# Kernel tuning notes

Hardware: AMD Instinct MI355X
Metric: run time of the kernel (lower is better)

Reference implementation:

```python
import jax, jax.numpy as jnp
import numpy as np

N_NODES = 50000
N_EDGES = 800000
IN_F, H_F, OUT_F = 512, 128, 64


def _graph_conv(x, W, b, src, dst, norm_src, norm_dst):
    # DGL GraphConv, norm='both': out = D_dst^-1/2 * A * (D_src^-1/2 * x) @ W + b
    # weight applied before aggregation (in_feats >= out_feats path) — math identical.
    h = (x * norm_src[:, None]) @ W                      # [N, out_f]
    agg = jax.ops.segment_sum(h[src], dst, num_segments=N_NODES)  # SpMM gather/scatter
    return agg * norm_dst[:, None] + b


def setup_inputs() -> dict:
    key = jax.random.key(0)
    ks = jax.random.split(key, 12)
    x = jax.random.normal(ks[0], (N_NODES, IN_F), dtype=jnp.float32)
    src = jax.random.randint(ks[1], (N_EDGES,), 0, N_NODES, dtype=jnp.int64)
    dst = jax.random.randint(ks[2], (N_EDGES,), 0, N_NODES, dtype=jnp.int64)

    def glorot(k, fan_in, fan_out):
        s = jnp.sqrt(6.0 / (fan_in + fan_out)).astype(jnp.float32)
        return jax.random.uniform(k, (fan_in, fan_out), jnp.float32, -s, s)

    return {
        'x': x, 'src': src, 'dst': dst,
        'W1': glorot(ks[3], IN_F, H_F), 'b1': jnp.zeros((H_F,), jnp.float32),
        'W2': glorot(ks[4], H_F, H_F), 'b2': jnp.zeros((H_F,), jnp.float32),
        'W3': glorot(ks[5], H_F, H_F), 'b3': jnp.zeros((H_F,), jnp.float32),
        'W4': glorot(ks[6], H_F, OUT_F), 'b4': jnp.zeros((OUT_F,), jnp.float32),
        'embedding_layer': 3,
    }


def reference(x, src, dst, W1, b1, W2, b2, W3, b3, W4, b4, embedding_layer):
    ones = jnp.ones((N_EDGES,), jnp.float32)
    out_deg = jnp.maximum(jax.ops.segment_sum(ones, src, num_segments=N_NODES), 1.0)
    in_deg = jnp.maximum(jax.ops.segment_sum(ones, dst, num_segments=N_NODES), 1.0)
    norm_src = jax.lax.rsqrt(out_deg)
    norm_dst = jax.lax.rsqrt(in_deg)

    h1 = jax.nn.relu(_graph_conv(x, W1, b1, src, dst, norm_src, norm_dst))
    h2 = jax.nn.relu(_graph_conv(h1, W2, b2, src, dst, norm_src, norm_dst))
    h3 = jax.nn.relu(_graph_conv(h2, W3, b3, src, dst, norm_src, norm_dst))
    h4 = _graph_conv(h3, W4, b4, src, dst, norm_src, norm_dst)

    hidden = [h1, h2, h3, h4][embedding_layer - 1]  # embedding_layer is a static int
    return (h4, hidden, x)
```

## Files before the change

kernel.cpp:

```cpp
#include <hip/hip_runtime.h>

#define N_NODES 50000
#define N_EDGES 800000
#define IN_F 512
#define H_F 128
#define OUT_F 64


__global__ void detect_kernel(const void* __restrict__ edges, int* __restrict__ flag) {
    if (threadIdx.x == 0 && blockIdx.x == 0) {
        const long long* p = (const long long*)edges;
        int is64 = 1;
        for (int k = 0; k < 256; k++) {
            long long v = p[k];
            if (v < 0 || v >= N_NODES) { is64 = 0; break; }
        }
        flag[0] = is64;
    }
}

__device__ __forceinline__ int edge_at(const void* __restrict__ p, int e, int is64) {
    return is64 ? (int)((const long long*)p)[e] : ((const int*)p)[e];
}

__global__ void count_kernel(const void* __restrict__ src, const void* __restrict__ dst,
                             int* __restrict__ cs, int* __restrict__ cd,
                             const int* __restrict__ flag) {
    int is64 = flag[0];
    int e = blockIdx.x * 256 + threadIdx.x;
    if (e < N_EDGES) {
        atomicAdd(&cs[edge_at(src, e, is64)], 1);
        atomicAdd(&cd[edge_at(dst, e, is64)], 1);
    }
}

__global__ void scan_kernel(const int* __restrict__ in, int* __restrict__ exc,
                            int* __restrict__ bsums, int n) {
    __shared__ int tmp[1024];
    int tid = threadIdx.x;
    int gid = blockIdx.x * 1024 + tid;
    int v = (gid < n) ? in[gid] : 0;
    tmp[tid] = v;
    __syncthreads();
    for (int off = 1; off < 1024; off <<= 1) {
        int t = (tid >= off) ? tmp[tid - off] : 0;
        __syncthreads();
        tmp[tid] += t;
        __syncthreads();
    }
    if (gid < n) exc[gid] = tmp[tid] - v;
    if (tid == 1023) bsums[blockIdx.x] = tmp[1023];
}

__global__ void finalize_kernel(const int* __restrict__ exc, const int* __restrict__ bexc,
                                int* __restrict__ rp, int* __restrict__ cur,
                                const int* __restrict__ cs, const int* __restrict__ cd,
                                float* __restrict__ ns, float* __restrict__ nd) {
    int i = blockIdx.x * 256 + threadIdx.x;
    if (i < N_NODES) {
        int v = exc[i] + bexc[i >> 10];
        rp[i] = v;
        cur[i] = v;
        if (i == 0) rp[N_NODES] = N_EDGES;
        ns[i] = 1.0f / sqrtf(fmaxf((float)cs[i], 1.0f));
        nd[i] = 1.0f / sqrtf(fmaxf((float)cd[i], 1.0f));
    }
}

__global__ void fill_kernel(const void* __restrict__ src, const void* __restrict__ dst,
                            int* __restrict__ cur, int* __restrict__ col,
                            const int* __restrict__ flag) {
    int is64 = flag[0];
    int e = blockIdx.x * 256 + threadIdx.x;
    if (e < N_EDGES) {
        int d = edge_at(dst, e, is64);
        int pos = atomicAdd(&cur[d], 1);
        col[pos] = edge_at(src, e, is64);
    }
}


__device__ __forceinline__ constexpr int swz(int f) { return f + (f >> 3); }

template <int N, int BM, bool COPY>
__global__ __launch_bounds__(256) void gemm_norm(const float* __restrict__ A, const float* __restrict__ W,
                                                 const float* __restrict__ norm, float* __restrict__ C,
                                                 int K, float* __restrict__ xc) {
    constexpr int TX = N / 8;
    constexpr int TY = 256 / TX;
    constexpr int RT = BM / TY;
    constexpr int NF4 = N / 4;
    constexpr int SA = BM + 4;
    constexpr int SW = (swz(NF4 - 1) + 1) * 4;
    constexpr int APT = BM * 32 / 4 / 256;
    constexpr int WPT = 32 * NF4 / 256;

    __shared__ float Ast[32 * SA];
    __shared__ float Ws[32 * SW];

    const int t = threadIdx.x;
    const int tx = t % TX, ty = t / TX;
    const int m0 = blockIdx.x * BM;
    const int KT = K / 32;

    float4 abuf[APT], wbuf[WPT];

    auto load_tile = [&](int k0) {
        #pragma unroll
        for (int p = 0; p < APT; p++) {
            int idx = t + p * 256;
            int r = idx >> 3;
            int c = (idx & 7) << 2;
            int row = m0 + r;
            abuf[p] = make_float4(0.f, 0.f, 0.f, 0.f);
            if (row < N_NODES) abuf[p] = *(const float4*)&A[(size_t)row * K + k0 + c];
        }
        #pragma unroll
        for (int p = 0; p < WPT; p++) {
            int idx = t + p * 256;
            int r = idx / NF4;
            int f = idx % NF4;
            wbuf[p] = *(const float4*)&W[(size_t)(k0 + r) * N + f * 4];
        }
    };
    auto store_tile = [&](int k0) {
        #pragma unroll
        for (int p = 0; p < APT; p++) {
            int idx = t + p * 256;
            int r = idx >> 3;
            int c = (idx & 7) << 2;
            Ast[(c + 0) * SA + r] = abuf[p].x;
            Ast[(c + 1) * SA + r] = abuf[p].y;
            Ast[(c + 2) * SA + r] = abuf[p].z;
            Ast[(c + 3) * SA + r] = abuf[p].w;
            if (COPY) {
                int row = m0 + r;
                if (row < N_NODES) *(float4*)&xc[(size_t)row * K + k0 + c] = abuf[p];
            }
        }
        #pragma unroll
        for (int p = 0; p < WPT; p++) {
            int idx = t + p * 256;
            int r = idx / NF4;
            int f = idx % NF4;
            *(float4*)&Ws[r * SW + swz(f) * 4] = wbuf[p];
        }
    };

    float acc[RT][8];
    #pragma unroll
    for (int i = 0; i < RT; i++)
        #pragma unroll
        for (int j = 0; j < 8; j++) acc[i][j] = 0.f;

    load_tile(0);
    store_tile(0);
    __syncthreads();

    for (int kt = 0; kt < KT; kt++) {
        if (kt + 1 < KT) load_tile((kt + 1) * 32);
        #pragma unroll 8
        for (int kk = 0; kk < 32; kk++) {
            float a[RT], w[8];
            #pragma unroll
            for (int r4 = 0; r4 < RT / 4; r4++)
                *(float4*)&a[r4 * 4] = *(const float4*)&Ast[kk * SA + ty * RT + r4 * 4];
            int f0 = tx * 2;
            *(float4*)&w[0] = *(const float4*)&Ws[kk * SW + (f0 + (f0 >> 3)) * 4];
            *(float4*)&w[4] = *(const float4*)&Ws[kk * SW + (f0 + 1 + ((f0 + 1) >> 3)) * 4];
            #pragma unroll
            for (int i = 0; i < RT; i++)
                #pragma unroll
                for (int j = 0; j < 8; j++) acc[i][j] = fmaf(a[i], w[j], acc[i][j]);
        }
        __syncthreads();
        if (kt + 1 < KT) {
            store_tile((kt + 1) * 32);
            __syncthreads();
        }
    }

    #pragma unroll
    for (int i = 0; i < RT; i++) {
        int row = m0 + ty * RT + i;
        if (row < N_NODES) {
            float s = norm[row];
            float4 o0 = make_float4(acc[i][0] * s, acc[i][1] * s, acc[i][2] * s, acc[i][3] * s);
            float4 o1 = make_float4(acc[i][4] * s, acc[i][5] * s, acc[i][6] * s, acc[i][7] * s);
            *(float4*)&C[(size_t)row * N + tx * 8] = o0;
            *(float4*)&C[(size_t)row * N + tx * 8 + 4] = o1;
        }
    }
}


template <int FEAT, bool RELU, bool HID>
__global__ __launch_bounds__(256) void spmm_kernel(
        const float* __restrict__ h, const int* __restrict__ rp,
        const int* __restrict__ col, const float* __restrict__ nd,
        const float* __restrict__ bias, float* __restrict__ out,
        float* __restrict__ hid, const int* __restrict__ emb, int layer) {
    int i = blockIdx.x * 4 + (threadIdx.x >> 6);
    i = __builtin_amdgcn_readfirstlane(i);
    if (i >= N_NODES) return;
    int lane = threadIdx.x & 63;
    int beg = rp[i], end = rp[i + 1];

    if constexpr (FEAT == 128) {
        float ax = 0.f, ay = 0.f;
        int e = beg;
        for (; e + 8 <= end; e += 8) {
            int c0 = col[e], c1 = col[e+1], c2 = col[e+2], c3 = col[e+3];
            int c4 = col[e+4], c5 = col[e+5], c6 = col[e+6], c7 = col[e+7];
            float2 v0 = *(const float2*)&h[(size_t)c0 * FEAT + lane * 2];
            float2 v1 = *(const float2*)&h[(size_t)c1 * FEAT + lane * 2];
            float2 v2 = *(const float2*)&h[(size_t)c2 * FEAT + lane * 2];
            float2 v3 = *(const float2*)&h[(size_t)c3 * FEAT + lane * 2];
            float2 v4 = *(const float2*)&h[(size_t)c4 * FEAT + lane * 2];
            float2 v5 = *(const float2*)&h[(size_t)c5 * FEAT + lane * 2];
            float2 v6 = *(const float2*)&h[(size_t)c6 * FEAT + lane * 2];
            float2 v7 = *(const float2*)&h[(size_t)c7 * FEAT + lane * 2];
            ax += (v0.x + v1.x) + (v2.x + v3.x) + ((v4.x + v5.x) + (v6.x + v7.x));
            ay += (v0.y + v1.y) + (v2.y + v3.y) + ((v4.y + v5.y) + (v6.y + v7.y));
        }
        for (; e < end; e++) {
            float2 v = *(const float2*)&h[(size_t)col[e] * FEAT + lane * 2];
            ax += v.x; ay += v.y;
        }
        float s = nd[i];
        float2 b = *(const float2*)&bias[lane * 2];
        float vx = fmaf(ax, s, b.x), vy = fmaf(ay, s, b.y);
        if (RELU) { vx = fmaxf(vx, 0.f); vy = fmaxf(vy, 0.f); }
        float2 o = make_float2(vx, vy);
        *(float2*)&out[(size_t)i * FEAT + lane * 2] = o;
        if (HID) {
            if (emb[0] == layer) *(float2*)&hid[(size_t)i * FEAT + lane * 2] = o;
        }
    } else {
        float acc = 0.f;
        int e = beg;
        for (; e + 8 <= end; e += 8) {
            int c0 = col[e], c1 = col[e+1], c2 = col[e+2], c3 = col[e+3];
            int c4 = col[e+4], c5 = col[e+5], c6 = col[e+6], c7 = col[e+7];
            float v0 = h[(size_t)c0 * FEAT + lane];
            float v1 = h[(size_t)c1 * FEAT + lane];
            float v2 = h[(size_t)c2 * FEAT + lane];
            float v3 = h[(size_t)c3 * FEAT + lane];
            float v4 = h[(size_t)c4 * FEAT + lane];
            float v5 = h[(size_t)c5 * FEAT + lane];
            float v6 = h[(size_t)c6 * FEAT + lane];
            float v7 = h[(size_t)c7 * FEAT + lane];
            acc += (v0 + v1) + (v2 + v3) + ((v4 + v5) + (v6 + v7));
        }
        for (; e < end; e++) acc += h[(size_t)col[e] * FEAT + lane];
        float v = fmaf(acc, nd[i], bias[lane]);
        if (RELU) v = fmaxf(v, 0.f);
        out[(size_t)i * FEAT + lane] = v;
        if (HID) {
            if (emb[0] == layer) hid[(size_t)i * FEAT + lane] = v;
        }
    }
}


extern "C" void kernel_launch(void* const* d_in, const int* in_sizes, int n_in,
                              void* d_out, int out_size, void* d_ws, size_t ws_size,
                              hipStream_t stream) {
    const float* x = (const float*)d_in[0];
    const void* src = d_in[1];
    const void* dst = d_in[2];
    const float* W1 = (const float*)d_in[3];  const float* b1 = (const float*)d_in[4];
    const float* W2 = (const float*)d_in[5];  const float* b2 = (const float*)d_in[6];
    const float* W3 = (const float*)d_in[7];  const float* b3 = (const float*)d_in[8];
    const float* W4 = (const float*)d_in[9];  const float* b4 = (const float*)d_in[10];
    const int* emb = (const int*)d_in[11];
    float* out = (float*)d_out;

    char* w = (char*)d_ws;
    int* cnt_src = (int*)w;  w += 51200 * 4;
    int* cnt_dst = (int*)w;  w += 51200 * 4;
    float* norm_src = (float*)w; w += 51200 * 4;
    float* norm_dst = (float*)w; w += 51200 * 4;
    int* exc = (int*)w;      w += 51200 * 4;
    int* bsums = (int*)w;    w += 1024 * 4;
    int* bexc = (int*)w;     w += 1024 * 4;
    int* bdummy = (int*)w;   w += 1024 * 4;
    int* dflag = (int*)w;    w += 1024 * 4;
    int* rp = (int*)w;       w += 51200 * 4;
    int* cur = (int*)w;      w += 51200 * 4;
    int* col = (int*)w;      w += 800768 * 4;
    float* gbuf = (float*)w; w += (size_t)6400000 * 4;
    float* hbuf = (float*)w; w += (size_t)6400000 * 4;

    hipMemsetAsync(cnt_src, 0, 2 * 51200 * 4, stream);
    detect_kernel<<<1, 64, 0, stream>>>(dst, dflag);
    count_kernel<<<3125, 256, 0, stream>>>(src, dst, cnt_src, cnt_dst, dflag);
    scan_kernel<<<49, 1024, 0, stream>>>(cnt_dst, exc, bsums, N_NODES);
    scan_kernel<<<1, 1024, 0, stream>>>(bsums, bexc, bdummy, 49);
    finalize_kernel<<<196, 256, 0, stream>>>(exc, bexc, rp, cur,
                                             cnt_src, cnt_dst, norm_src, norm_dst);
    fill_kernel<<<3125, 256, 0, stream>>>(src, dst, cur, col, dflag);

    const int GB64 = (N_NODES + 63) / 64;
    const int GB128 = (N_NODES + 127) / 128;
    const int SB = (N_NODES + 3) / 4;
    float* hid = out + (size_t)N_NODES * OUT_F;
    float* xcopy = hid + (size_t)N_NODES * H_F;

    gemm_norm<128, 64, true><<<GB64, 256, 0, stream>>>(x, W1, norm_src, gbuf, IN_F, xcopy);
    spmm_kernel<128, true, true><<<SB, 256, 0, stream>>>(gbuf, rp, col, norm_dst, b1, hbuf, hid, emb, 1);

    gemm_norm<128, 64, false><<<GB64, 256, 0, stream>>>(hbuf, W2, norm_src, gbuf, H_F, nullptr);
    spmm_kernel<128, true, true><<<SB, 256, 0, stream>>>(gbuf, rp, col, norm_dst, b2, hbuf, hid, emb, 2);

    gemm_norm<128, 64, false><<<GB64, 256, 0, stream>>>(hbuf, W3, norm_src, gbuf, H_F, nullptr);
    spmm_kernel<128, true, true><<<SB, 256, 0, stream>>>(gbuf, rp, col, norm_dst, b3, hbuf, hid, emb, 3);

    gemm_norm<64, 128, false><<<GB128, 256, 0, stream>>>(hbuf, W4, norm_src, gbuf, H_F, nullptr);
    spmm_kernel<64, false, false><<<SB, 256, 0, stream>>>(gbuf, rp, col, norm_dst, b4, out, nullptr, nullptr, 0);
}
```

Measured before the change: 754.3 us.

## Replace FP32 SIMT GEMM with split-bf16 MFMA GEMM and pre-swizzled weights

Replaces the scalar FP32 tiled GEMM with an MFMA-based kernel that represents each FP32 value as a bf16 hi/lo pair and uses three bf16 MFMAs per tile to approximate FP32 precision. Weights are converted once per call into hi/lo bf16 arrays laid out in the MFMA operand fragment order. Activations are split on the fly and staged through a small shared-memory tile. This trades FP32 FMA throughput for matrix-core throughput, at the cost of reduced precision and a smaller 32-row tile that does less data reuse and syncs twice per K step.

Result: faster. 648.6 us (-14.0%).

```diff
diff --git a/kernel.cpp b/kernel.cpp
--- a/kernel.cpp
+++ b/kernel.cpp
@@ -80,115 +80,113 @@
 }
 
 
-__device__ __forceinline__ constexpr int swz(int f) { return f + (f >> 3); }
-
-template <int N, int BM, bool COPY>
-__global__ __launch_bounds__(256) void gemm_norm(const float* __restrict__ A, const float* __restrict__ W,
-                                                 const float* __restrict__ norm, float* __restrict__ C,
-                                                 int K, float* __restrict__ xc) {
-    constexpr int TX = N / 8;
-    constexpr int TY = 256 / TX;
-    constexpr int RT = BM / TY;
-    constexpr int NF4 = N / 4;
-    constexpr int SA = BM + 4;
-    constexpr int SW = (swz(NF4 - 1) + 1) * 4;
-    constexpr int APT = BM * 32 / 4 / 256;
-    constexpr int WPT = 32 * NF4 / 256;
-
-    __shared__ float Ast[32 * SA];
-    __shared__ float Ws[32 * SW];
+__device__ __forceinline__ ushort f2bf(float f) {
+    unsigned int u = __float_as_uint(f);
+    unsigned int r = u + 0x7FFFu + ((u >> 16) & 1u);
+    return (ushort)(r >> 16);
+}
+__device__ __forceinline__ float bf2f(ushort h) {
+    return __uint_as_float(((unsigned int)h) << 16);
+}
+
+
+__global__ void wconv_kernel(const float* __restrict__ W1, const float* __restrict__ W2,
+                             const float* __restrict__ W3, const float* __restrict__ W4,
+                             ushort* __restrict__ hi, ushort* __restrict__ lo) {
+    int id = blockIdx.x * 256 + threadIdx.x;
+    const float* Wp; int N, rel, base;
+    if (id < 65536)       { Wp = W1; N = 128; rel = id;          base = 0; }
+    else if (id < 81920)  { Wp = W2; N = 128; rel = id - 65536;  base = 65536; }
+    else if (id < 98304)  { Wp = W3; N = 128; rel = id - 81920;  base = 81920; }
+    else if (id < 106496) { Wp = W4; N = 64;  rel = id - 98304;  base = 98304; }
+    else return;
+    int k = rel / N, n = rel % N;
+    float v = Wp[rel];
+    int NS = N >> 4;
+    int kt = k >> 5, kk = k & 31, ns = n >> 4;
+    int lane = (n & 15) + 16 * (kk >> 3), j = kk & 7;
+    int dst = base + ((kt * NS + ns) * 64 + lane) * 8 + j;
+    ushort h = f2bf(v);
+    hi[dst] = h;
+    lo[dst] = f2bf(v - bf2f(h));
+}
+
+
+typedef __attribute__((ext_vector_type(8))) short short8v;
+typedef __attribute__((ext_vector_type(4))) float floatx4;
+
+template <int N, bool COPY>
+__global__ __launch_bounds__(256) void gemm_mfma(const float* __restrict__ A,
+                                                 const ushort* __restrict__ Whi,
+                                                 const ushort* __restrict__ Wlo,
+                                                 const float* __restrict__ norm,
+                                                 float* __restrict__ C, int K,
+                                                 float* __restrict__ xc) {
+    constexpr int NS = N / 16;
+    constexpr int NSW = NS / 2;
+
+    __shared__ ushort Ahi[2][64][8];
+    __shared__ ushort Alo[2][64][8];
 
     const int t = threadIdx.x;
-    const int tx = t % TX, ty = t / TX;
-    const int m0 = blockIdx.x * BM;
-    const int KT = K / 32;
-
-    float4 abuf[APT], wbuf[WPT];
-
-    auto load_tile = [&](int k0) {
+    const int w = t >> 6, lane = t & 63;
+    const int rowsub = w & 1, nsb = (w >> 1) * NSW;
+    const int m0 = blockIdx.x * 32;
+    const int sr = t >> 3;
+    const int sc = (t & 7) << 2;
+    const int ss = sr >> 4;
+    const int sl = (sr & 15) + 16 * (sc >> 3);
+    const int sj = sc & 7;
+    const int row = m0 + sr;
+    const int KT = K >> 5;
+
+    floatx4 acc[NSW];
+    #pragma unroll
+    for (int q = 0; q < NSW; q++) acc[q] = (floatx4)(0.0f);
+
+    for (int kt = 0; kt < KT; kt++) {
+        short8v bhi[NSW], blo[NSW];
         #pragma unroll
-        for (int p = 0; p < APT; p++) {
-            int idx = t + p * 256;
-            int r = idx >> 3;
-            int c = (idx & 7) << 2;
-            int row = m0 + r;
-            abuf[p] = make_float4(0.f, 0.f, 0.f, 0.f);
-            if (row < N_NODES) abuf[p] = *(const float4*)&A[(size_t)row * K + k0 + c];
-        }
+        for (int q = 0; q < NSW; q++) {
+            size_t fb = ((size_t)(kt * NS + nsb + q) * 64 + lane) * 8;
+            bhi[q] = *(const short8v*)&Whi[fb];
+            blo[q] = *(const short8v*)&Wlo[fb];
+        }
+        float4 v = make_float4(0.f, 0.f, 0.f, 0.f);
+        if (row < N_NODES) {
+            v = *(const float4*)&A[(size_t)row * K + kt * 32 + sc];
+            if (COPY) *(float4*)&xc[(size_t)row * K + kt * 32 + sc] = v;
+        }
+        ushort4 h4, l4;
+        h4.x = f2bf(v.x); l4.x = f2bf(v.x - bf2f(h4.x));
+        h4.y = f2bf(v.y); l4.y = f2bf(v.y - bf2f(h4.y));
+        h4.z = f2bf(v.z); l4.z = f2bf(v.z - bf2f(h4.z));
+        h4.w = f2bf(v.w); l4.w = f2bf(v.w - bf2f(h4.w));
+        *(ushort4*)&Ahi[ss][sl][sj] = h4;
+        *(ushort4*)&Alo[ss][sl][sj] = l4;
+        __syncthreads();
+
+        short8v ah = *(const short8v*)&Ahi[rowsub][lane][0];
+        short8v al = *(const short8v*)&Alo[rowsub][lane][0];
         #pragma unroll
-        for (int p = 0; p < WPT; p++) {
-            int idx = t + p * 256;
-            int r = idx / NF4;
-            int f = idx % NF4;
-            wbuf[p] = *(const float4*)&W[(size_t)(k0 + r) * N + f * 4];
-        }
-    };
-    auto store_tile = [&](int k0) {
-        #pragma unroll
-        for (int p = 0; p < APT; p++) {
-            int idx = t + p * 256;
-            int r = idx >> 3;
-            int c = (idx & 7) << 2;
-            Ast[(c + 0) * SA + r] = abuf[p].x;
-            Ast[(c + 1) * SA + r] = abuf[p].y;
-            Ast[(c + 2) * SA + r] = abuf[p].z;
-            Ast[(c + 3) * SA + r] = abuf[p].w;
-            if (COPY) {
-                int row = m0 + r;
-                if (row < N_NODES) *(float4*)&xc[(size_t)row * K + k0 + c] = abuf[p];
+        for (int q = 0; q < NSW; q++) {
+            acc[q] = __builtin_amdgcn_mfma_f32_16x16x32_bf16(ah, bhi[q], acc[q], 0, 0, 0);
+            acc[q] = __builtin_amdgcn_mfma_f32_16x16x32_bf16(ah, blo[q], acc[q], 0, 0, 0);
+            acc[q] = __builtin_amdgcn_mfma_f32_16x16x32_bf16(al, bhi[q], acc[q], 0, 0, 0);
+        }
+        __syncthreads();
+    }
+
+    #pragma unroll
+    for (int rr = 0; rr < 4; rr++) {
+        int gr = m0 + rowsub * 16 + (lane >> 4) * 4 + rr;
+        if (gr < N_NODES) {
+            float s = norm[gr];
+            #pragma unroll
+            for (int q = 0; q < NSW; q++) {
+                int gc = (nsb + q) * 16 + (lane & 15);
+                C[(size_t)gr * N + gc] = acc[q][rr] * s;
             }
-        }
-        #pragma unroll
-        for (int p = 0; p < WPT; p++) {
-            int idx = t + p * 256;
-            int r = idx / NF4;
-            int f = idx % NF4;
-            *(float4*)&Ws[r * SW + swz(f) * 4] = wbuf[p];
-        }
-    };
-
-    float acc[RT][8];
-    #pragma unroll
-    for (int i = 0; i < RT; i++)
-        #pragma unroll
-        for (int j = 0; j < 8; j++) acc[i][j] = 0.f;
-
-    load_tile(0);
-    store_tile(0);
-    __syncthreads();
-
-    for (int kt = 0; kt < KT; kt++) {
-        if (kt + 1 < KT) load_tile((kt + 1) * 32);
-        #pragma unroll 8
-        for (int kk = 0; kk < 32; kk++) {
-            float a[RT], w[8];
-            #pragma unroll
-            for (int r4 = 0; r4 < RT / 4; r4++)
-                *(float4*)&a[r4 * 4] = *(const float4*)&Ast[kk * SA + ty * RT + r4 * 4];
-            int f0 = tx * 2;
-            *(float4*)&w[0] = *(const float4*)&Ws[kk * SW + (f0 + (f0 >> 3)) * 4];
-            *(float4*)&w[4] = *(const float4*)&Ws[kk * SW + (f0 + 1 + ((f0 + 1) >> 3)) * 4];
-            #pragma unroll
-            for (int i = 0; i < RT; i++)
-                #pragma unroll
-                for (int j = 0; j < 8; j++) acc[i][j] = fmaf(a[i], w[j], acc[i][j]);
-        }
-        __syncthreads();
-        if (kt + 1 < KT) {
-            store_tile((kt + 1) * 32);
-            __syncthreads();
-        }
-    }
-
-    #pragma unroll
-    for (int i = 0; i < RT; i++) {
-        int row = m0 + ty * RT + i;
-        if (row < N_NODES) {
-            float s = norm[row];
-            float4 o0 = make_float4(acc[i][0] * s, acc[i][1] * s, acc[i][2] * s, acc[i][3] * s);
-            float4 o1 = make_float4(acc[i][4] * s, acc[i][5] * s, acc[i][6] * s, acc[i][7] * s);
-            *(float4*)&C[(size_t)row * N + tx * 8] = o0;
-            *(float4*)&C[(size_t)row * N + tx * 8 + 4] = o1;
         }
     }
 }
@@ -291,6 +289,8 @@
     int* col = (int*)w;      w += 800768 * 4;
     float* gbuf = (float*)w; w += (size_t)6400000 * 4;
     float* hbuf = (float*)w; w += (size_t)6400000 * 4;
+    ushort* whi = (ushort*)w; w += 106496 * 2;
+    ushort* wlo = (ushort*)w; w += 106496 * 2;
 
     hipMemsetAsync(cnt_src, 0, 2 * 51200 * 4, stream);
     detect_kernel<<<1, 64, 0, stream>>>(dst, dflag);
@@ -300,22 +300,22 @@
     finalize_kernel<<<196, 256, 0, stream>>>(exc, bexc, rp, cur,
                                              cnt_src, cnt_dst, norm_src, norm_dst);
     fill_kernel<<<3125, 256, 0, stream>>>(src, dst, cur, col, dflag);
-
-    const int GB64 = (N_NODES + 63) / 64;
-    const int GB128 = (N_NODES + 127) / 128;
+    wconv_kernel<<<416, 256, 0, stream>>>(W1, W2, W3, W4, whi, wlo);
+
+    const int GM = (N_NODES + 31) / 32;
     const int SB = (N_NODES + 3) / 4;
     float* hid = out + (size_t)N_NODES * OUT_F;
     float* xcopy = hid + (size_t)N_NODES * H_F;
 
-    gemm_norm<128, 64, true><<<GB64, 256, 0, stream>>>(x, W1, norm_src, gbuf, IN_F, xcopy);
+    gemm_mfma<128, true><<<GM, 256, 0, stream>>>(x, whi, wlo, norm_src, gbuf, IN_F, xcopy);
     spmm_kernel<128, true, true><<<SB, 256, 0, stream>>>(gbuf, rp, col, norm_dst, b1, hbuf, hid, emb, 1);
 
-    gemm_norm<128, 64, false><<<GB64, 256, 0, stream>>>(hbuf, W2, norm_src, gbuf, H_F, nullptr);
+    gemm_mfma<128, false><<<GM, 256, 0, stream>>>(hbuf, whi + 65536, wlo + 65536, norm_src, gbuf, H_F, nullptr);
     spmm_kernel<128, true, true><<<SB, 256, 0, stream>>>(gbuf, rp, col, norm_dst, b2, hbuf, hid, emb, 2);
 
-    gemm_norm<128, 64, false><<<GB64, 256, 0, stream>>>(hbuf, W3, norm_src, gbuf, H_F, nullptr);
+    gemm_mfma<128, false><<<GM, 256, 0, stream>>>(hbuf, whi + 81920, wlo + 81920, norm_src, gbuf, H_F, nullptr);
     spmm_kernel<128, true, true><<<SB, 256, 0, stream>>>(gbuf, rp, col, norm_dst, b3, hbuf, hid, emb, 3);
 
-    gemm_norm<64, 128, false><<<GB128, 256, 0, stream>>>(hbuf, W4, norm_src, gbuf, H_F, nullptr);
+    gemm_mfma<64, false><<<GM, 256, 0, stream>>>(hbuf, whi + 98304, wlo + 98304, norm_src, gbuf, H_F, nullptr);
     spmm_kernel<64, false, false><<<SB, 256, 0, stream>>>(gbuf, rp, col, norm_dst, b4, out, nullptr, nullptr, 0);
 }
```
